# Kernel tuning notes

Hardware: AMD Instinct MI355X
Metric: run time of the kernel (lower is better)

Reference implementation:

```python
import jax, jax.numpy as jnp
import numpy as np

N = 50000          # nodes
M_UND = 500000     # undirected edges -> E = 2*M_UND directed messages
Q = 16             # num_groups
MAX_ITER = 10
BP_MAX_DIFF = 0.01


def setup_inputs() -> dict:
    key = jax.random.key(0)
    k1, k2, k3, k4 = jax.random.split(key, 4)
    u = jax.random.randint(k1, (M_UND,), 0, N)
    v = jax.random.randint(k2, (M_UND,), 0, N)
    # each undirected edge (u,v) yields directed messages u->v and v->u
    src = jnp.concatenate([u, v]).astype(jnp.int32)
    dst = jnp.concatenate([v, u]).astype(jnp.int32)
    rev = jnp.concatenate([jnp.arange(M_UND) + M_UND, jnp.arange(M_UND)]).astype(jnp.int32)
    psi0 = jax.random.uniform(k3, (N, Q), dtype=jnp.float32)
    psi0 = psi0 / psi0.sum(1, keepdims=True)
    msg0 = jax.random.uniform(k4, (2 * M_UND, Q), dtype=jnp.float32)
    msg0 = msg0 / msg0.sum(1, keepdims=True)
    c = 2.0 * M_UND / N  # mean degree
    beta = jnp.float32(np.log(Q / np.sqrt(c - 1.0) + 1.0))  # beta_ast init
    return dict(src=src, dst=dst, rev=rev, psi0=psi0, msg0=msg0, beta=beta, n_nodes=N)


def _bp_forward(src, dst, rev, psi0, msg0, beta, n_nodes):
    q = psi0.shape[1]
    n_edges = msg0.shape[0]
    mean_w = float(n_edges) / (float(n_nodes) * float(n_nodes))  # W.mean() for 0/1 weights
    expb_m1 = jnp.exp(beta) - 1.0
    h0 = (-beta * mean_w * psi0).sum(0)  # external field, shape [q]

    def step(carry, _):
        msg, psi, h, done = carry
        # S_e = 1 + psi_{src->dst} * (e^{beta*w} - 1), w == 1
        logS = jnp.log1p(msg * expb_m1)                                    # [E, q]
        node_log = jax.ops.segment_sum(logS, dst, num_segments=n_nodes)    # prod over incoming, log-domain
        # cavity update: message i->j uses all incoming to i except j->i (rev edge)
        new_msg = jax.nn.softmax(node_log[src] - logS[rev] + h, axis=-1)   # exp(h)*prod, normalized
        diff = jnp.max(jnp.abs(jax.lax.stop_gradient(new_msg) -
                               jax.lax.stop_gradient(msg)).sum(-1))
        logS2 = jnp.log1p(new_msg * expb_m1)
        node_log2 = jax.ops.segment_sum(logS2, dst, num_segments=n_nodes)
        new_psi = jax.nn.softmax(node_log2 + h, axis=-1)                    # marginals
        new_h = (-beta * mean_w * new_psi).sum(0)
        # freeze state once converged (mirrors early-return on max_diff < bp_max_diff)
        msg = jnp.where(done, msg, new_msg)
        psi = jnp.where(done, psi, new_psi)
        h = jnp.where(done, h, new_h)
        done = done | (diff < BP_MAX_DIFF)
        return (msg, psi, h, done), diff

    (msg, psi, h, done), _ = jax.lax.scan(
        step, (msg0, psi0, h0, jnp.array(False)), None, length=MAX_ITER)

    # soft modularity: (1/2m) sum_e psi_i . psi_j - sum_g (sum_i d_i psi_ig / 2m)^2
    m2 = float(n_edges)  # total directed edge weight (= 2m for unit weights)
    deg = jax.ops.segment_sum(jnp.ones((n_edges,), psi.dtype), dst, num_segments=n_nodes)
    edge_term = jnp.einsum('eq,eq->', psi[src], psi[dst]) / m2
    deg_term = jnp.sum((jnp.einsum('n,nq->q', deg, psi) / m2) ** 2)
    modularity = edge_term - deg_term
    # group-balance regularizer, scaled by sqrt(q) as in forward()
    reg = jnp.sum((psi.sum(0) / float(n_nodes) - 1.0 / q) ** 2) * np.sqrt(q)
    # mean per-node entropy of marginals, normalized by log(q)
    entropy_loss = jnp.mean(-jnp.sum(psi * jnp.log(psi + 1e-12), axis=-1)) / np.log(q)
    return psi, reg, entropy_loss, modularity


def reference(src, dst, rev, psi0, msg0, beta, n_nodes):
    return _bp_forward(src, dst, rev, psi0, msg0, beta, n_nodes)
```

## Files before the change

kernel.cpp:

```cpp
#include <hip/hip_runtime.h>

#define Q 16
#define SCAN_B 256

__device__ __forceinline__ float wsum(float v){
  #pragma unroll
  for(int o=32;o;o>>=1) v += __shfl_xor(v,o);
  return v;
}
__device__ __forceinline__ float wmaxr(float v){
  #pragma unroll
  for(int o=32;o;o>>=1) v = fmaxf(v,__shfl_xor(v,o));
  return v;
}

__global__ void __launch_bounds__(256, 4) k_edge16C(
    const int* __restrict__ src, const int* __restrict__ dst,
    const int* __restrict__ ipos,
    float* msgC, const float* __restrict__ nl, const float* __restrict__ hc,
    const float* __restrict__ betap,
    float* __restrict__ diffpart, const int* __restrict__ donep, int M)
{
  if (*donep) return;
  const float eb = __expf(*betap) - 1.0f;
  const int q = threadIdx.x & 15;
  const float hq = hc[q];
  const int grp  = (blockIdx.x*blockDim.x + threadIdx.x) >> 4;
  const int ngrp = (gridDim.x*blockDim.x) >> 4;
  float dloc = 0.0f;
  int p = grp;
  for (; p + ngrp < M; p += 2*ngrp){
    const int pA = p, pB = p + ngrp;
    const int uA = src[pA], vA = dst[pA];
    const int uB = src[pB], vB = dst[pB];
    const int a0 = ipos[pA], a1 = ipos[pA + M];
    const int b0 = ipos[pB], b1 = ipos[pB + M];
    const float mA0 = msgC[(size_t)a0*Q + q], mA1 = msgC[(size_t)a1*Q + q];
    const float mB0 = msgC[(size_t)b0*Q + q], mB1 = msgC[(size_t)b1*Q + q];
    const float nuA = nl[(size_t)uA*Q + q],  nvA = nl[(size_t)vA*Q + q];
    const float nuB = nl[(size_t)uB*Q + q],  nvB = nl[(size_t)vB*Q + q];
    float tA0 = nuA - __logf(fmaf(mA1, eb, 1.0f)) + hq;
    float tA1 = nvA - __logf(fmaf(mA0, eb, 1.0f)) + hq;
    float tB0 = nuB - __logf(fmaf(mB1, eb, 1.0f)) + hq;
    float tB1 = nvB - __logf(fmaf(mB0, eb, 1.0f)) + hq;
    float xA0=tA0, xA1=tA1, xB0=tB0, xB1=tB1;
    #pragma unroll
    for (int o=1;o<16;o<<=1){
      xA0=fmaxf(xA0,__shfl_xor(xA0,o)); xA1=fmaxf(xA1,__shfl_xor(xA1,o));
      xB0=fmaxf(xB0,__shfl_xor(xB0,o)); xB1=fmaxf(xB1,__shfl_xor(xB1,o));
    }
    const float eA0=__expf(tA0-xA0), eA1=__expf(tA1-xA1);
    const float eB0=__expf(tB0-xB0), eB1=__expf(tB1-xB1);
    float sA0=eA0, sA1=eA1, sB0=eB0, sB1=eB1;
    #pragma unroll
    for (int o=1;o<16;o<<=1){
      sA0+=__shfl_xor(sA0,o); sA1+=__shfl_xor(sA1,o);
      sB0+=__shfl_xor(sB0,o); sB1+=__shfl_xor(sB1,o);
    }
    const float nA0=eA0/sA0, nA1=eA1/sA1, nB0=eB0/sB0, nB1=eB1/sB1;
    float dA0=fabsf(nA0-mA0), dA1=fabsf(nA1-mA1);
    float dB0=fabsf(nB0-mB0), dB1=fabsf(nB1-mB1);
    #pragma unroll
    for (int o=1;o<16;o<<=1){
      dA0+=__shfl_xor(dA0,o); dA1+=__shfl_xor(dA1,o);
      dB0+=__shfl_xor(dB0,o); dB1+=__shfl_xor(dB1,o);
    }
    dloc = fmaxf(dloc, fmaxf(fmaxf(dA0,dA1), fmaxf(dB0,dB1)));
    msgC[(size_t)a0*Q + q] = nA0;  msgC[(size_t)a1*Q + q] = nA1;
    msgC[(size_t)b0*Q + q] = nB0;  msgC[(size_t)b1*Q + q] = nB1;
  }
  if (p < M){
    const int u = src[p], v = dst[p];
    const int i0 = ipos[p], i1 = ipos[p + M];
    const float m0 = msgC[(size_t)i0*Q + q], m1 = msgC[(size_t)i1*Q + q];
    const float nu = nl[(size_t)u*Q + q],   nv = nl[(size_t)v*Q + q];
    float t0 = nu - __logf(fmaf(m1, eb, 1.0f)) + hq;
    float t1 = nv - __logf(fmaf(m0, eb, 1.0f)) + hq;
    float x0=t0, x1=t1;
    #pragma unroll
    for (int o=1;o<16;o<<=1){
      x0=fmaxf(x0,__shfl_xor(x0,o)); x1=fmaxf(x1,__shfl_xor(x1,o));
    }
    const float e0=__expf(t0-x0), e1=__expf(t1-x1);
    float s0=e0, s1=e1;
    #pragma unroll
    for (int o=1;o<16;o<<=1){ s0+=__shfl_xor(s0,o); s1+=__shfl_xor(s1,o); }
    const float n0=e0/s0, n1=e1/s1;
    float d0=fabsf(n0-m0), d1=fabsf(n1-m1);
    #pragma unroll
    for (int o=1;o<16;o<<=1){ d0+=__shfl_xor(d0,o); d1+=__shfl_xor(d1,o); }
    dloc = fmaxf(dloc, fmaxf(d0,d1));
    msgC[(size_t)i0*Q + q] = n0;  msgC[(size_t)i1*Q + q] = n1;
  }
  __shared__ float smx[4];
  float wm = wmaxr(dloc);
  if ((threadIdx.x & 63) == 0) smx[threadIdx.x>>6] = wm;
  __syncthreads();
  if (threadIdx.x == 0)
    diffpart[blockIdx.x] = fmaxf(fmaxf(smx[0],smx[1]), fmaxf(smx[2],smx[3]));
}

__global__ void __launch_bounds__(256, 4) k_gatherC(
    const float* __restrict__ msgC, const int* __restrict__ offs,
    float* __restrict__ nl, const float* __restrict__ hc,
    float* __restrict__ psi, const float* __restrict__ betap,
    const int* __restrict__ donep, float* __restrict__ hpart,
    int N, int mode)
{
  if (mode && *donep) return;
  const int wid = threadIdx.x >> 6;
  const int n = blockIdx.x*4 + wid;
  const float eb = __expf(*betap) - 1.0f;
  const int lane = threadIdx.x & 63;
  const int sub = lane >> 4, q16 = lane & 15;
  int start = 0, end = 0;
  if (n < N){ start = offs[n]; end = offs[n+1]; }
  float acc = 0.0f;
  int i = start + sub;
  for (; i + 4 < end; i += 8){
    const float x0 = msgC[(size_t)i*Q + q16];
    const float x1 = msgC[(size_t)(i+4)*Q + q16];
    acc += __logf(fmaf(x0, eb, 1.0f)) + __logf(fmaf(x1, eb, 1.0f));
  }
  if (i < end) acc += __logf(fmaf(msgC[(size_t)i*Q + q16], eb, 1.0f));
  acc += __shfl_xor(acc, 16);
  acc += __shfl_xor(acc, 32);
  if (n < N && sub == 0) nl[(size_t)n*Q + q16] = acc;
  if (!mode) return;
  float t = acc + hc[q16];
  float m = t;
  #pragma unroll
  for (int o=1;o<16;o<<=1) m = fmaxf(m, __shfl_xor(m,o));
  float ex = __expf(t-m);
  float s = ex;
  #pragma unroll
  for (int o=1;o<16;o<<=1) s += __shfl_xor(s,o);
  const float pq = ex/s;
  if (n < N && sub == 0) psi[(size_t)n*Q + q16] = pq;
  __shared__ float smh[4][17];
  if (sub == 0) smh[wid][q16] = (n < N) ? pq : 0.0f;
  __syncthreads();
  if (threadIdx.x < Q)
    hpart[(size_t)blockIdx.x*Q + threadIdx.x] =
      smh[0][threadIdx.x]+smh[1][threadIdx.x]+smh[2][threadIdx.x]+smh[3][threadIdx.x];
}

__global__ void __launch_bounds__(256) k_hred2(
    const float* __restrict__ hpart, int nrows,
    float* __restrict__ hpart2, int gH,
    const float* __restrict__ diffpart, int nbd,
    float* __restrict__ h, int* __restrict__ donep,
    int* __restrict__ cnt,
    const float* __restrict__ betap, float mean_w)
{
  if (*donep) return;
  const int t = threadIdx.x, g = t>>4, q = t&15;
  __shared__ float sm[16][17];
  {
    const int base = blockIdx.x*256;
    const int lim = min(base+256, nrows);
    float s = 0.0f;
    for (int r = base+g; r < lim; r += 16) s += hpart[(size_t)r*Q + q];
    sm[g][q] = s; __syncthreads();
    if (t < Q){
      float tot = 0.0f;
      #pragma unroll
      for (int i=0;i<16;i++) tot += sm[i][t];
      hpart2[(size_t)blockIdx.x*Q + t] = tot;
    }
  }
  __shared__ int amLast;
  __threadfence();
  if (t == 0) amLast = (atomicAdd(cnt, 1) == gH-1);
  __syncthreads();
  if (!amLast) return;
  {
    float s = 0.0f;
    for (int b = g; b < gH; b += 16) s += hpart2[(size_t)b*Q + q];
    __syncthreads();
    sm[g][q] = s; __syncthreads();
    if (t < Q){
      float tot = 0.0f;
      #pragma unroll
      for (int i=0;i<16;i++) tot += sm[i][t];
      h[t] = -(*betap) * mean_w * tot;
    }
  }
  float m = 0.0f;
  for (int i = t; i < nbd; i += 256) m = fmaxf(m, diffpart[i]);
  m = wmaxr(m);
  __shared__ float red[4];
  if ((t & 63) == 0) red[t>>6] = m;
  __syncthreads();
  if (t == 0 &&
      fmaxf(fmaxf(red[0],red[1]), fmaxf(red[2],red[3])) < 0.01f) *donep = 1;
}

__global__ void __launch_bounds__(256) k_h_part(
    const float* __restrict__ psi, float* __restrict__ hpart, int N)
{
  const int n = blockIdx.x*blockDim.x + threadIdx.x;
  float pv[Q];
  if (n < N) {
    const float4* a = (const float4*)(psi + (size_t)n*Q);
    #pragma unroll
    for (int i=0;i<4;i++){ float4 t=a[i]; pv[4*i]=t.x; pv[4*i+1]=t.y; pv[4*i+2]=t.z; pv[4*i+3]=t.w; }
  } else {
    #pragma unroll
    for (int q=0;q<Q;q++) pv[q]=0.0f;
  }
  __shared__ float sm[4][Q];
  const int wid = threadIdx.x>>6, lane = threadIdx.x&63;
  #pragma unroll
  for (int q=0;q<Q;q++){
    float s = wsum(pv[q]);
    if (lane == 0) sm[wid][q] = s;
  }
  __syncthreads();
  if (threadIdx.x < Q)
    hpart[(size_t)blockIdx.x*Q + threadIdx.x] =
      sm[0][threadIdx.x]+sm[1][threadIdx.x]+sm[2][threadIdx.x]+sm[3][threadIdx.x];
}

__global__ void __launch_bounds__(256) k_hfin(
    const float* __restrict__ hpart, float* __restrict__ h,
    const float* __restrict__ betap, int nb, float mean_w)
{
  const int t = threadIdx.x, g = t>>4, q = t&15;
  float s = 0.0f;
  for (int b = g; b < nb; b += 16) s += hpart[(size_t)b*Q + q];
  __shared__ float sm[16][17];
  sm[g][q] = s; __syncthreads();
  if (t < Q){
    float tot = 0.0f;
    #pragma unroll
    for (int i=0;i<16;i++) tot += sm[i][t];
    h[t] = -(*betap) * mean_w * tot;
  }
}

__global__ void __launch_bounds__(256) k_deg(
    const int* __restrict__ dst, int* __restrict__ deg, int E)
{
  const int e = blockIdx.x*blockDim.x + threadIdx.x;
  if (e < E) atomicAdd(&deg[dst[e]], 1);
}

__global__ void __launch_bounds__(SCAN_B) k_scan1(
    const int* __restrict__ deg, int* __restrict__ offs,
    int* __restrict__ bsum, int N)
{
  __shared__ int sm[SCAN_B];
  const int i = blockIdx.x*SCAN_B + threadIdx.x;
  const int v = (i<N) ? deg[i] : 0;
  sm[threadIdx.x] = v; __syncthreads();
  #pragma unroll
  for (int o=1;o<SCAN_B;o<<=1){
    int t = (threadIdx.x>=o) ? sm[threadIdx.x-o] : 0;
    __syncthreads();
    sm[threadIdx.x] += t;
    __syncthreads();
  }
  if (i<N) offs[i] = sm[threadIdx.x] - v;
  if (threadIdx.x==SCAN_B-1) bsum[blockIdx.x] = sm[threadIdx.x];
}

__global__ void __launch_bounds__(SCAN_B) k_scan2(int* __restrict__ bsum, int nb)
{
  __shared__ int sm[SCAN_B];
  const int v = (threadIdx.x<nb) ? bsum[threadIdx.x] : 0;
  sm[threadIdx.x] = v; __syncthreads();
  #pragma unroll
  for (int o=1;o<SCAN_B;o<<=1){
    int t = (threadIdx.x>=o) ? sm[threadIdx.x-o] : 0;
    __syncthreads();
    sm[threadIdx.x] += t;
    __syncthreads();
  }
  if (threadIdx.x<nb) bsum[threadIdx.x] = sm[threadIdx.x] - v;
}

__global__ void __launch_bounds__(SCAN_B) k_scan3(
    int* __restrict__ offs, int* __restrict__ cursor,
    const int* __restrict__ bsum, int N, int E)
{
  const int i = blockIdx.x*SCAN_B + threadIdx.x;
  if (i<N){
    const int o = offs[i] + bsum[blockIdx.x];
    offs[i] = o; cursor[i] = o;
  }
  if (i==0) offs[N] = E;
}

__global__ void __launch_bounds__(256) k_fillCS(
    const int* __restrict__ dst, int* __restrict__ cursor,
    const float* __restrict__ msg0, float* __restrict__ msgC,
    int* __restrict__ ipos, int E)
{
  const int e = blockIdx.x*blockDim.x + threadIdx.x;
  if (e >= E) return;
  const int ip = atomicAdd(&cursor[dst[e]], 1);
  ipos[e] = ip;
  const float4* s = (const float4*)(msg0 + (size_t)e*Q);
  float4* d = (float4*)(msgC + (size_t)ip*Q);
  float4 x0=s[0], x1=s[1], x2=s[2], x3=s[3];
  d[0]=x0; d[1]=x1; d[2]=x2; d[3]=x3;
}

__global__ void __launch_bounds__(256) k_stats(
    const int* __restrict__ src, const int* __restrict__ dst,
    const float* __restrict__ psi, const int* __restrict__ deg,
    float* __restrict__ colpart, float* __restrict__ degpart,
    float* __restrict__ entpart, float* __restrict__ edgepart,
    int* __restrict__ cnt, float* __restrict__ out,
    int M, int N, int NQ, float m2, int gS)
{
  const int t = threadIdx.x;
  const int lane = t & 63, wid = t >> 6;
  float ed = 0.0f;
  for (int p = blockIdx.x*256 + t; p < M; p += gS*256){
    const int u = src[p], v = dst[p];
    const float4* a = (const float4*)(psi + (size_t)u*Q);
    const float4* b = (const float4*)(psi + (size_t)v*Q);
    float d = 0.0f;
    #pragma unroll
    for (int i=0;i<4;i++){
      float4 x=a[i], y=b[i];
      d += x.x*y.x + x.y*y.y + x.z*y.z + x.w*y.w;
    }
    ed += 2.0f*d;
  }
  float ca[Q], da[Q]; float ea = 0.0f;
  #pragma unroll
  for (int q=0;q<Q;q++){ ca[q]=0.0f; da[q]=0.0f; }
  for (int n = blockIdx.x*256 + t; n < N; n += gS*256){
    const float4* a = (const float4*)(psi + (size_t)n*Q);
    float pv[Q];
    #pragma unroll
    for (int i=0;i<4;i++){ float4 x=a[i]; pv[4*i]=x.x; pv[4*i+1]=x.y; pv[4*i+2]=x.z; pv[4*i+3]=x.w; }
    const float dg = (float)deg[n];
    #pragma unroll
    for (int q=0;q<Q;q++){
      ca[q] += pv[q];
      da[q] += pv[q]*dg;
      ea    -= pv[q]*__logf(pv[q]+1e-12f);
    }
  }
  __shared__ float smc[4][17], smd[4][17];
  __shared__ float sme[4], smeE[4];
  __shared__ float smg[16][17], smg2[16][17];
  __shared__ int amL;
  #pragma unroll
  for (int q=0;q<Q;q++){
    float s  = wsum(ca[q]);
    float s2 = wsum(da[q]);
    if (lane == 0){ smc[wid][q]=s; smd[wid][q]=s2; }
  }
  float se = wsum(ea);
  float sed = wsum(ed);
  if (lane == 0){ sme[wid]=se; smeE[wid]=sed; }
  __syncthreads();
  if (t < Q){
    colpart[(size_t)blockIdx.x*Q+t] = smc[0][t]+smc[1][t]+smc[2][t]+smc[3][t];
    degpart[(size_t)blockIdx.x*Q+t] = smd[0][t]+smd[1][t]+smd[2][t]+smd[3][t];
  }
  if (t == 0){
    entpart[blockIdx.x]  = sme[0]+sme[1]+sme[2]+sme[3];
    edgepart[blockIdx.x] = smeE[0]+smeE[1]+smeE[2]+smeE[3];
  }
  __threadfence();
  if (t == 0) amL = (atomicAdd(cnt, 1) == gS-1);
  __syncthreads();
  if (!amL) return;
  {
    const int g = t>>4, qq = t&15;
    float cs=0.0f, ds=0.0f;
    for (int r = g; r < gS; r += 16){
      cs += colpart[(size_t)r*Q + qq];
      ds += degpart[(size_t)r*Q + qq];
    }
    smg[g][qq] = cs; smg2[g][qq] = ds;
    __syncthreads();
    float colq=0.0f, degq=0.0f;
    if (t < Q){
      #pragma unroll
      for (int i=0;i<16;i++){ colq += smg[i][t]; degq += smg2[i][t]; }
    }
    float es=0.0f, en=0.0f;
    for (int i=t; i<gS; i+=256){ es += edgepart[i]; en += entpart[i]; }
    es = wsum(es); en = wsum(en);
    if (lane == 0){ smeE[wid]=es; sme[wid]=en; }
    __syncthreads();
    if (t < Q){ smg[0][t] = colq; smg2[0][t] = degq; }
    __syncthreads();
    if (t == 0){
      const float edge_total = smeE[0]+smeE[1]+smeE[2]+smeE[3];
      const float ent_total  = sme[0]+sme[1]+sme[2]+sme[3];
      float reg = 0.0f, dt = 0.0f;
      for (int i=0;i<Q;i++){
        float d = smg[0][i]/(float)N - 1.0f/(float)Q; reg += d*d;
        float s = smg2[0][i]/m2; dt += s*s;
      }
      out[NQ+0] = reg * 4.0f;
      out[NQ+1] = ent_total/(float)N / 2.7725887222397811f;
      out[NQ+2] = edge_total/m2 - dt;
    }
  }
}

extern "C" void kernel_launch(void* const* d_in, const int* in_sizes, int n_in,
                              void* d_out, int out_size, void* d_ws, size_t ws_size,
                              hipStream_t stream)
{
  const int*   src   = (const int*)  d_in[0];
  const int*   dst   = (const int*)  d_in[1];
  const float* psi0  = (const float*)d_in[3];
  const float* msg0  = (const float*)d_in[4];
  const float* betap = (const float*)d_in[5];

  const int E  = in_sizes[0];
  const int M  = E/2;
  const int NQ = in_sizes[3];
  const int N  = NQ/Q;
  const float mean_w = (float)((double)E/((double)N*(double)N));
  const float m2 = (float)E;

  const int B = 256;
  const int gE = (E+B-1)/B, gN = (N+B-1)/B;
  const int nb = (N+SCAN_B-1)/SCAN_B;
  const int nbE = 2048;
  const int gW = (N+3)/4;
  const int gH = (gW+255)/256;
  const int gS = 256;
  const int HPROWS = (gW > gN ? gW : gN);

  char* w = (char*)d_ws;
  float* msgC    = (float*)w; w += (size_t)E*Q*sizeof(float);
  float* nl      = (float*)w; w += (size_t)NQ*sizeof(float);
  int*   ipos    = (int*)  w; w += (size_t)E*sizeof(int);
  int*   offs    = (int*)  w; w += (size_t)(N+16)*sizeof(int);
  int*   cursor  = (int*)  w; w += (size_t)(N+16)*sizeof(int);
  int*   bsum    = (int*)  w; w += 256*sizeof(int);
  float* hpart   = (float*)w; w += (size_t)HPROWS*Q*sizeof(float);
  float* hpart2  = (float*)w; w += (size_t)(gH+4)*Q*sizeof(float);
  float* diffpart= (float*)w; w += (size_t)nbE*sizeof(float);
  float* edgepart= (float*)w; w += (size_t)gS*sizeof(float);
  float* colpart = (float*)w; w += (size_t)gS*Q*sizeof(float);
  float* degpart = (float*)w; w += (size_t)gS*Q*sizeof(float);
  float* entpart = (float*)w; w += (size_t)gS*sizeof(float);
  int*   deg     = (int*)  w; w += (size_t)(N+16)*sizeof(int);
  float* h       = (float*)w; w += 16*sizeof(float);
  int*   donep   = (int*)  w; w += 4*sizeof(int);
  int*   cnt     = (int*)  w; w += 16*sizeof(int);
  int*   cnts    = (int*)  w; w += 4*sizeof(int);

  float* psi = (float*)d_out;

  const size_t small_bytes = (size_t)((char*)w - (char*)deg);
  hipMemsetAsync(deg, 0, small_bytes, stream);

  k_h_part <<<gN,B,0,stream>>>(psi0, hpart, N);
  k_hfin   <<<1, B,0,stream>>>(hpart, h, betap, gN, mean_w);
  k_deg    <<<gE,B,0,stream>>>(dst, deg, E);
  k_scan1  <<<nb,SCAN_B,0,stream>>>(deg, offs, bsum, N);
  k_scan2  <<<1, SCAN_B,0,stream>>>(bsum, nb);
  k_scan3  <<<nb,SCAN_B,0,stream>>>(offs, cursor, bsum, N, E);
  k_fillCS <<<gE,B,0,stream>>>(dst, cursor, msg0, msgC, ipos, E);
  k_gatherC<<<gW,B,0,stream>>>(msgC, offs, nl, h, psi, betap, donep, hpart, N, 0);

  for (int k=0; k<10; ++k) {
    k_edge16C<<<nbE,B,0,stream>>>(src, dst, ipos, msgC, nl, h, betap,
                                  diffpart, donep, M);
    k_gatherC<<<gW,B,0,stream>>>(msgC, offs, nl, h, psi, betap, donep,
                                 hpart, N, 1);
    k_hred2  <<<gH,B,0,stream>>>(hpart, gW, hpart2, gH, diffpart, nbE,
                                 h, donep, &cnt[k], betap, mean_w);
  }

  k_stats<<<gS,B,0,stream>>>(src, dst, psi, deg, colpart, degpart,
                             entpart, edgepart, cnts, psi, M, N, NQ, m2, gS);
}
```

Baseline: 1.020 ms.

## Store messages in edge order and gather through an edge-id CSR index

Messages are no longer permuted into destination-sorted (CSR) order. The edge kernel now reads and writes each message pair contiguously at its edge index, using msg0 directly on the first iteration. The per-node gather instead goes through a new eid indirection array, and the initial scatter-copy of msg0 is dropped. This moves the random-access traffic from the edge kernel's reads and scattered writes to the gather's reads, and it also removes the edge kernel's two-edge unrolling, which may reduce the number of memory loads in flight.

```diff
diff --git a/kernel.cpp b/kernel.cpp
--- a/kernel.cpp
+++ b/kernel.cpp
@@ -14,10 +14,10 @@
   return v;
 }
 
-__global__ void __launch_bounds__(256, 4) k_edge16C(
+__global__ void __launch_bounds__(256, 4) k_edge16(
     const int* __restrict__ src, const int* __restrict__ dst,
-    const int* __restrict__ ipos,
-    float* msgC, const float* __restrict__ nl, const float* __restrict__ hc,
+    const float* msg_in, float* msg_out,
+    const float* __restrict__ nl, const float* __restrict__ hc,
     const float* __restrict__ betap,
     float* __restrict__ diffpart, const int* __restrict__ donep, int M)
 {
@@ -28,69 +28,39 @@
   const int grp  = (blockIdx.x*blockDim.x + threadIdx.x) >> 4;
   const int ngrp = (gridDim.x*blockDim.x) >> 4;
   float dloc = 0.0f;
-  int p = grp;
-  for (; p + ngrp < M; p += 2*ngrp){
-    const int pA = p, pB = p + ngrp;
-    const int uA = src[pA], vA = dst[pA];
-    const int uB = src[pB], vB = dst[pB];
-    const int a0 = ipos[pA], a1 = ipos[pA + M];
-    const int b0 = ipos[pB], b1 = ipos[pB + M];
-    const float mA0 = msgC[(size_t)a0*Q + q], mA1 = msgC[(size_t)a1*Q + q];
-    const float mB0 = msgC[(size_t)b0*Q + q], mB1 = msgC[(size_t)b1*Q + q];
-    const float nuA = nl[(size_t)uA*Q + q],  nvA = nl[(size_t)vA*Q + q];
-    const float nuB = nl[(size_t)uB*Q + q],  nvB = nl[(size_t)vB*Q + q];
-    float tA0 = nuA - __logf(fmaf(mA1, eb, 1.0f)) + hq;
-    float tA1 = nvA - __logf(fmaf(mA0, eb, 1.0f)) + hq;
-    float tB0 = nuB - __logf(fmaf(mB1, eb, 1.0f)) + hq;
-    float tB1 = nvB - __logf(fmaf(mB0, eb, 1.0f)) + hq;
-    float xA0=tA0, xA1=tA1, xB0=tB0, xB1=tB1;
+  for (int p = grp; p < M; p += ngrp){
+    const int u = src[p], v = dst[p];
+    const float muv = msg_in[(size_t)p*Q + q];
+    const float mvu = msg_in[((size_t)p + (size_t)M)*Q + q];
+    const float nlu = nl[(size_t)u*Q + q];
+    const float nlv = nl[(size_t)v*Q + q];
+    const float lsuv = __logf(fmaf(muv, eb, 1.0f));
+    const float lsvu = __logf(fmaf(mvu, eb, 1.0f));
+    float tuv = nlu - lsvu + hq;
+    float tvu = nlv - lsuv + hq;
+    float m1 = tuv, m2 = tvu;
     #pragma unroll
     for (int o=1;o<16;o<<=1){
-      xA0=fmaxf(xA0,__shfl_xor(xA0,o)); xA1=fmaxf(xA1,__shfl_xor(xA1,o));
-      xB0=fmaxf(xB0,__shfl_xor(xB0,o)); xB1=fmaxf(xB1,__shfl_xor(xB1,o));
-    }
-    const float eA0=__expf(tA0-xA0), eA1=__expf(tA1-xA1);
-    const float eB0=__expf(tB0-xB0), eB1=__expf(tB1-xB1);
-    float sA0=eA0, sA1=eA1, sB0=eB0, sB1=eB1;
+      m1 = fmaxf(m1, __shfl_xor(m1,o));
+      m2 = fmaxf(m2, __shfl_xor(m2,o));
+    }
+    const float e1 = __expf(tuv-m1), e2 = __expf(tvu-m2);
+    float s1 = e1, s2 = e2;
     #pragma unroll
     for (int o=1;o<16;o<<=1){
-      sA0+=__shfl_xor(sA0,o); sA1+=__shfl_xor(sA1,o);
-      sB0+=__shfl_xor(sB0,o); sB1+=__shfl_xor(sB1,o);
-    }
-    const float nA0=eA0/sA0, nA1=eA1/sA1, nB0=eB0/sB0, nB1=eB1/sB1;
-    float dA0=fabsf(nA0-mA0), dA1=fabsf(nA1-mA1);
-    float dB0=fabsf(nB0-mB0), dB1=fabsf(nB1-mB1);
+      s1 += __shfl_xor(s1,o);
+      s2 += __shfl_xor(s2,o);
+    }
+    const float nuv = e1/s1, nvu = e2/s2;
+    float d1 = fabsf(nuv-muv), d2 = fabsf(nvu-mvu);
     #pragma unroll
     for (int o=1;o<16;o<<=1){
-      dA0+=__shfl_xor(dA0,o); dA1+=__shfl_xor(dA1,o);
-      dB0+=__shfl_xor(dB0,o); dB1+=__shfl_xor(dB1,o);
-    }
-    dloc = fmaxf(dloc, fmaxf(fmaxf(dA0,dA1), fmaxf(dB0,dB1)));
-    msgC[(size_t)a0*Q + q] = nA0;  msgC[(size_t)a1*Q + q] = nA1;
-    msgC[(size_t)b0*Q + q] = nB0;  msgC[(size_t)b1*Q + q] = nB1;
-  }
-  if (p < M){
-    const int u = src[p], v = dst[p];
-    const int i0 = ipos[p], i1 = ipos[p + M];
-    const float m0 = msgC[(size_t)i0*Q + q], m1 = msgC[(size_t)i1*Q + q];
-    const float nu = nl[(size_t)u*Q + q],   nv = nl[(size_t)v*Q + q];
-    float t0 = nu - __logf(fmaf(m1, eb, 1.0f)) + hq;
-    float t1 = nv - __logf(fmaf(m0, eb, 1.0f)) + hq;
-    float x0=t0, x1=t1;
-    #pragma unroll
-    for (int o=1;o<16;o<<=1){
-      x0=fmaxf(x0,__shfl_xor(x0,o)); x1=fmaxf(x1,__shfl_xor(x1,o));
-    }
-    const float e0=__expf(t0-x0), e1=__expf(t1-x1);
-    float s0=e0, s1=e1;
-    #pragma unroll
-    for (int o=1;o<16;o<<=1){ s0+=__shfl_xor(s0,o); s1+=__shfl_xor(s1,o); }
-    const float n0=e0/s0, n1=e1/s1;
-    float d0=fabsf(n0-m0), d1=fabsf(n1-m1);
-    #pragma unroll
-    for (int o=1;o<16;o<<=1){ d0+=__shfl_xor(d0,o); d1+=__shfl_xor(d1,o); }
-    dloc = fmaxf(dloc, fmaxf(d0,d1));
-    msgC[(size_t)i0*Q + q] = n0;  msgC[(size_t)i1*Q + q] = n1;
+      d1 += __shfl_xor(d1,o);
+      d2 += __shfl_xor(d2,o);
+    }
+    dloc = fmaxf(dloc, fmaxf(d1,d2));
+    msg_out[(size_t)p*Q + q] = nuv;
+    msg_out[((size_t)p + (size_t)M)*Q + q] = nvu;
   }
   __shared__ float smx[4];
   float wm = wmaxr(dloc);
@@ -100,8 +70,9 @@
     diffpart[blockIdx.x] = fmaxf(fmaxf(smx[0],smx[1]), fmaxf(smx[2],smx[3]));
 }
 
-__global__ void __launch_bounds__(256, 4) k_gatherC(
-    const float* __restrict__ msgC, const int* __restrict__ offs,
+__global__ void __launch_bounds__(256, 4) k_gather(
+    const float* __restrict__ msg, const int* __restrict__ offs,
+    const int* __restrict__ eid,
     float* __restrict__ nl, const float* __restrict__ hc,
     float* __restrict__ psi, const float* __restrict__ betap,
     const int* __restrict__ donep, float* __restrict__ hpart,
@@ -118,11 +89,13 @@
   float acc = 0.0f;
   int i = start + sub;
   for (; i + 4 < end; i += 8){
-    const float x0 = msgC[(size_t)i*Q + q16];
-    const float x1 = msgC[(size_t)(i+4)*Q + q16];
+    const int e0 = eid[i], e1 = eid[i+4];
+    const float x0 = msg[(size_t)e0*Q + q16];
+    const float x1 = msg[(size_t)e1*Q + q16];
     acc += __logf(fmaf(x0, eb, 1.0f)) + __logf(fmaf(x1, eb, 1.0f));
   }
-  if (i < end) acc += __logf(fmaf(msgC[(size_t)i*Q + q16], eb, 1.0f));
+  if (i < end)
+    acc += __logf(fmaf(msg[(size_t)eid[i]*Q + q16], eb, 1.0f));
   acc += __shfl_xor(acc, 16);
   acc += __shfl_xor(acc, 32);
   if (n < N && sub == 0) nl[(size_t)n*Q + q16] = acc;
@@ -292,19 +265,15 @@
   if (i==0) offs[N] = E;
 }
 
-__global__ void __launch_bounds__(256) k_fillCS(
+__global__ void __launch_bounds__(256) k_fill(
     const int* __restrict__ dst, int* __restrict__ cursor,
-    const float* __restrict__ msg0, float* __restrict__ msgC,
-    int* __restrict__ ipos, int E)
+    int* __restrict__ eid, int E)
 {
   const int e = blockIdx.x*blockDim.x + threadIdx.x;
-  if (e >= E) return;
-  const int ip = atomicAdd(&cursor[dst[e]], 1);
-  ipos[e] = ip;
-  const float4* s = (const float4*)(msg0 + (size_t)e*Q);
-  float4* d = (float4*)(msgC + (size_t)ip*Q);
-  float4 x0=s[0], x1=s[1], x2=s[2], x3=s[3];
-  d[0]=x0; d[1]=x1; d[2]=x2; d[3]=x3;
+  if (e < E){
+    const int p = atomicAdd(&cursor[dst[e]], 1);
+    eid[p] = e;
+  }
 }
 
 __global__ void __launch_bounds__(256) k_stats(
@@ -435,9 +404,9 @@
   const int HPROWS = (gW > gN ? gW : gN);
 
   char* w = (char*)d_ws;
-  float* msgC    = (float*)w; w += (size_t)E*Q*sizeof(float);
+  float* msgA    = (float*)w; w += (size_t)E*Q*sizeof(float);
   float* nl      = (float*)w; w += (size_t)NQ*sizeof(float);
-  int*   ipos    = (int*)  w; w += (size_t)E*sizeof(int);
+  int*   eid     = (int*)  w; w += (size_t)E*sizeof(int);
   int*   offs    = (int*)  w; w += (size_t)(N+16)*sizeof(int);
   int*   cursor  = (int*)  w; w += (size_t)(N+16)*sizeof(int);
   int*   bsum    = (int*)  w; w += 256*sizeof(int);
@@ -459,22 +428,24 @@
   const size_t small_bytes = (size_t)((char*)w - (char*)deg);
   hipMemsetAsync(deg, 0, small_bytes, stream);
 
-  k_h_part <<<gN,B,0,stream>>>(psi0, hpart, N);
-  k_hfin   <<<1, B,0,stream>>>(hpart, h, betap, gN, mean_w);
-  k_deg    <<<gE,B,0,stream>>>(dst, deg, E);
-  k_scan1  <<<nb,SCAN_B,0,stream>>>(deg, offs, bsum, N);
-  k_scan2  <<<1, SCAN_B,0,stream>>>(bsum, nb);
-  k_scan3  <<<nb,SCAN_B,0,stream>>>(offs, cursor, bsum, N, E);
-  k_fillCS <<<gE,B,0,stream>>>(dst, cursor, msg0, msgC, ipos, E);
-  k_gatherC<<<gW,B,0,stream>>>(msgC, offs, nl, h, psi, betap, donep, hpart, N, 0);
+  k_h_part<<<gN,B,0,stream>>>(psi0, hpart, N);
+  k_hfin  <<<1, B,0,stream>>>(hpart, h, betap, gN, mean_w);
+  k_deg   <<<gE,B,0,stream>>>(dst, deg, E);
+  k_scan1 <<<nb,SCAN_B,0,stream>>>(deg, offs, bsum, N);
+  k_scan2 <<<1, SCAN_B,0,stream>>>(bsum, nb);
+  k_scan3 <<<nb,SCAN_B,0,stream>>>(offs, cursor, bsum, N, E);
+  k_fill  <<<gE,B,0,stream>>>(dst, cursor, eid, E);
+  k_gather<<<gW,B,0,stream>>>(msg0, offs, eid, nl, h, psi, betap, donep,
+                              hpart, N, 0);
 
   for (int k=0; k<10; ++k) {
-    k_edge16C<<<nbE,B,0,stream>>>(src, dst, ipos, msgC, nl, h, betap,
-                                  diffpart, donep, M);
-    k_gatherC<<<gW,B,0,stream>>>(msgC, offs, nl, h, psi, betap, donep,
-                                 hpart, N, 1);
-    k_hred2  <<<gH,B,0,stream>>>(hpart, gW, hpart2, gH, diffpart, nbE,
-                                 h, donep, &cnt[k], betap, mean_w);
+    const float* mc = (k==0) ? msg0 : msgA;
+    k_edge16<<<nbE,B,0,stream>>>(src, dst, mc, msgA, nl, h, betap,
+                                 diffpart, donep, M);
+    k_gather<<<gW,B,0,stream>>>(msgA, offs, eid, nl, h, psi, betap, donep,
+                                hpart, N, 1);
+    k_hred2 <<<gH,B,0,stream>>>(hpart, gW, hpart2, gH, diffpart, nbE,
+                                h, donep, &cnt[k], betap, mean_w);
   }
 
   k_stats<<<gS,B,0,stream>>>(src, dst, psi, deg, colpart, degpart,
```

After: 1.084 ms. +6.2%, slower.
